# Kernel tuning notes

Measured on AMD Instinct MI355X. Metric: run time of the kernel, lower is better.

Reference implementation:

```python
import jax, jax.numpy as jnp
import numpy as np

EMB = 300
NUM_LAYERS = 5
NUM_GRAPHS = 1024
NUM_JUNCTIONS = 8192
TEMP = 0.04
EPS = 1e-5
SELF_LOOP_BOND_TYPE = 4


def gcn_conv(x, edge_index, edge_attr, W, b, ee1, ee2):
    # pretrain-gnns GCNConv: add self-loops (bond type 4, direction 0),
    # degree-normalized add aggregation of (x_src + edge_emb).
    N = x.shape[0]
    loop = jnp.arange(N, dtype=edge_index.dtype)
    src = jnp.concatenate([edge_index[0], loop])
    dst = jnp.concatenate([edge_index[1], loop])
    bt = jnp.concatenate([edge_attr[:, 0], jnp.full((N,), SELF_LOOP_BOND_TYPE, edge_attr.dtype)])
    bd = jnp.concatenate([edge_attr[:, 1], jnp.zeros((N,), edge_attr.dtype)])
    eemb = ee1[bt] + ee2[bd]                                   # [E+N, D]
    deg = jax.ops.segment_sum(jnp.ones(src.shape, x.dtype), src, num_segments=N)
    dinv = jnp.where(deg > 0, 1.0 / jnp.sqrt(jnp.maximum(deg, 1e-12)), 0.0)
    norm = dinv[src] * dinv[dst]                               # [E+N]
    h = x @ W.T + b                                            # [N, D]
    msg = norm[:, None] * (h[src] + eemb)                      # gather + fuse
    return jax.ops.segment_sum(msg, dst, num_segments=N)      # scatter-add


def batchnorm(h, gamma, beta):
    mu = h.mean(0)
    var = h.var(0)
    return gamma * (h - mu) / jnp.sqrt(var + EPS) + beta


def gnn_encoder(x, edge_index, edge_attr, ae1, ae2, W, b, ee1, ee2, gamma, beta):
    h = ae1[x[:, 0]] + ae2[x[:, 1]]
    for l in range(NUM_LAYERS):
        h = gcn_conv(h, edge_index, edge_attr, W[l], b[l], ee1[l], ee2[l])
        h = batchnorm(h, gamma[l], beta[l])
        if l < NUM_LAYERS - 1:
            h = jax.nn.relu(h)
    return h


def junction_encoder(h, jW, jb, jee1, jee2):
    # SuperEncoder is called with empty edge_index -> only self-loops.
    empty_ei = jnp.zeros((2, 0), jnp.int32)
    empty_ea = jnp.zeros((0, 2), jnp.int32)
    h = jax.nn.relu(gcn_conv(h, empty_ei, empty_ea, jW[0], jb[0], jee1[0], jee2[0]))
    return gcn_conv(h, empty_ei, empty_ea, jW[1], jb[1], jee1[1], jee2[1])


def mean_pool(h, ids, num):
    s = jax.ops.segment_sum(h, ids, num_segments=num)
    c = jax.ops.segment_sum(jnp.ones((h.shape[0],), h.dtype), ids, num_segments=num)
    return s / jnp.maximum(c, 1.0)[:, None]


def l2norm(h):
    return h / jnp.maximum(jnp.linalg.norm(h, axis=1, keepdims=True), 1e-12)


def setup_inputs() -> dict:
    key = jax.random.key(0)
    ks = jax.random.split(key, 32)
    N, E = 200000, 400000
    inp = {
        'batch_x': jax.random.randint(ks[0], (N, 2), 0, 3, jnp.int32),
        'batch_edge_index': jax.random.randint(ks[1], (2, E), 0, N, jnp.int32),
        'batch_edge_attr': jax.random.randint(ks[2], (E, 2), 0, 3, jnp.int32),
        'batch_graph_ids': jax.random.randint(ks[3], (N,), 0, NUM_GRAPHS, jnp.int32),
        'frag_x': jax.random.randint(ks[4], (N, 2), 0, 3, jnp.int32),
        'frag_edge_index': jax.random.randint(ks[5], (2, E), 0, N, jnp.int32),
        'frag_edge_attr': jax.random.randint(ks[6], (E, 2), 0, 3, jnp.int32),
        'frag_junction_ids': jax.random.randint(ks[7], (N,), 0, NUM_JUNCTIONS, jnp.int32),
        'junction_graph_ids': jax.random.randint(ks[8], (NUM_JUNCTIONS,), 0, NUM_GRAPHS, jnp.int32),
        'junction_mask': jax.random.uniform(ks[9], (NUM_JUNCTIONS,), jnp.float32),
    }
    s = 0.05
    inp.update({
        'atom_emb1': jax.random.normal(ks[10], (120, EMB), jnp.float32) * s,
        'atom_emb2': jax.random.normal(ks[11], (3, EMB), jnp.float32) * s,
        'gnn_W': jax.random.normal(ks[12], (NUM_LAYERS, EMB, EMB), jnp.float32) * s,
        'gnn_b': jnp.zeros((NUM_LAYERS, EMB), jnp.float32),
        'gnn_ee1': jax.random.normal(ks[13], (NUM_LAYERS, 6, EMB), jnp.float32) * s,
        'gnn_ee2': jax.random.normal(ks[14], (NUM_LAYERS, 3, EMB), jnp.float32) * s,
        'bn_gamma': jnp.ones((NUM_LAYERS, EMB), jnp.float32),
        'bn_beta': jnp.zeros((NUM_LAYERS, EMB), jnp.float32),
        'jct_W': jax.random.normal(ks[15], (2, EMB, EMB), jnp.float32) * s,
        'jct_b': jnp.zeros((2, EMB), jnp.float32),
        'jct_ee1': jax.random.normal(ks[16], (2, 6, EMB), jnp.float32) * s,
        'jct_ee2': jax.random.normal(ks[17], (2, 3, EMB), jnp.float32) * s,
        'mask_embedding': jax.random.normal(ks[18], (EMB,), jnp.float32),
    })
    return inp


def reference(batch_x, batch_edge_index, batch_edge_attr, batch_graph_ids,
              frag_x, frag_edge_index, frag_edge_attr, frag_junction_ids,
              junction_graph_ids, junction_mask,
              atom_emb1, atom_emb2, gnn_W, gnn_b, gnn_ee1, gnn_ee2,
              bn_gamma, bn_beta, jct_W, jct_b, jct_ee1, jct_ee2, mask_embedding):
    # branch 0: whole molecules
    h = gnn_encoder(batch_x, batch_edge_index, batch_edge_attr,
                    atom_emb1, atom_emb2, gnn_W, gnn_b, gnn_ee1, gnn_ee2, bn_gamma, bn_beta)
    g = mean_pool(h, batch_graph_ids, NUM_GRAPHS)
    f0 = l2norm(junction_encoder(g, jct_W, jct_b, jct_ee1, jct_ee2))
    # branch 1: fragments -> junction nodes, masked overwrite, pooled per graph
    h = gnn_encoder(frag_x, frag_edge_index, frag_edge_attr,
                    atom_emb1, atom_emb2, gnn_W, gnn_b, gnn_ee1, gnn_ee2, bn_gamma, bn_beta)
    j = mean_pool(h, frag_junction_ids, NUM_JUNCTIONS)
    j = jnp.where(junction_mask[:, None] > 0.5, mask_embedding[None, :], j)
    j = junction_encoder(j, jct_W, jct_b, jct_ee1, jct_ee2)
    f1 = l2norm(mean_pool(j, junction_graph_ids, NUM_GRAPHS))
    logits = (f0 @ f1.T) / TEMP
    return logits
```

## Files before the change

### kernel.cpp

```cpp
#include <hip/hip_runtime.h>
#include <math.h>

#define EMBD 300
#define HROW 304
#define LDF  304
#define KEXT 320
#define BCH  80
#define BSTR 40
#define TS2  312
#define SPR  608
#define NTAB 24
#define CE(a,b) (((a)+(b)-1)/(b))

typedef _Float16 h16;
typedef __attribute__((ext_vector_type(8))) _Float16 half8;
typedef __attribute__((ext_vector_type(4))) float f32x4;

__global__ void k_diag(float* out, int n, float v){
  int i = blockIdx.x*256 + threadIdx.x;
  if (i < n) out[i] = v;
}
__global__ void k_init_deg(int* __restrict__ deg, int* __restrict__ cnts, int N){
  int i = blockIdx.x*256 + threadIdx.x;
  if (i < N){ deg[i] = 0; cnts[i] = 1; }
}
__global__ void k_count_both(const int* __restrict__ ei, int E,
                             int* __restrict__ deg, int* __restrict__ cnts){
  int e = blockIdx.x*256 + threadIdx.x;
  if (e < E){
    atomicAdd(&deg[ei[e]], 1);
    atomicAdd(&cnts[ei[E + e]], 1);
  }
}
__global__ void k_dinv(const int* __restrict__ deg, float* __restrict__ dinv, int N){
  int i = blockIdx.x*256 + threadIdx.x;
  if (i < N) dinv[i] = 1.0f / sqrtf((float)(deg[i] + 1));
}
__global__ void k_count_ids(const int* __restrict__ ids, int n, int* __restrict__ counts){
  int i = blockIdx.x*256 + threadIdx.x;
  if (i < n) atomicAdd(&counts[ids[i]], 1);
}
__global__ void k_scan_block(const int* __restrict__ in, int M, int* __restrict__ out, int* __restrict__ bsum){
  __shared__ int s[256];
  int t = threadIdx.x, i = blockIdx.x*256 + t;
  int v = (i < M) ? in[i] : 0;
  s[t] = v; __syncthreads();
  for (int off = 1; off < 256; off <<= 1){
    int x = (t >= off) ? s[t-off] : 0;
    __syncthreads();
    s[t] += x;
    __syncthreads();
  }
  if (i < M) out[i] = s[t] - v;
  if (t == 255) bsum[blockIdx.x] = s[255];
}
__global__ void k_scan_sums(int* __restrict__ bsum, int B){
  __shared__ int s[1024];
  int t = threadIdx.x;
  int v = (t < B) ? bsum[t] : 0;
  s[t] = v; __syncthreads();
  for (int off = 1; off < 1024; off <<= 1){
    int x = (t >= off) ? s[t-off] : 0;
    __syncthreads();
    s[t] += x;
    __syncthreads();
  }
  if (t < B) bsum[t] = s[t] - v;
}
__global__ void k_scan_add(int* __restrict__ out, const int* __restrict__ bsum, int M){
  int i = blockIdx.x*256 + threadIdx.x;
  if (i < M) out[i] += bsum[blockIdx.x];
}
__global__ void k_fill_edges(const int* __restrict__ ei, const int* __restrict__ ea, int E, int N,
                             const int* __restrict__ offs, int* __restrict__ cur, int* __restrict__ entries){
  int e = blockIdx.x*256 + threadIdx.x;
  if (e < E){
    int s  = ei[e];
    int d  = ei[E + e];
    int bt = ea[2*e], bd = ea[2*e + 1];
    int pos = offs[d] + atomicAdd(&cur[d], 1);
    entries[pos] = s | (bt << 20) | (bd << 23);
  } else if (e < E + N){
    int i = e - E;
    int pos = offs[i] + atomicAdd(&cur[i], 1);
    entries[pos] = i | (4 << 20);
  }
}
__global__ void k_fill_rows(const int* __restrict__ ids, int n, const int* __restrict__ offs,
                            int* __restrict__ cur, int* __restrict__ entries){
  int i = blockIdx.x*256 + threadIdx.x;
  if (i < n){
    int g = ids[i];
    int pos = offs[g] + atomicAdd(&cur[g], 1);
    entries[pos] = i;
  }
}

__global__ void k_htab(const float* __restrict__ ae1, const float* __restrict__ ae2,
                       h16* __restrict__ htab){
  int p = blockIdx.x;
  int a = p / 3, b = p % 3;
  int t = threadIdx.x;
  h16* d = htab + (size_t)p*HROW;
  for (int c = t; c < HROW; c += 256)
    d[c] = (c < EMBD) ? (h16)(ae1[(size_t)a*EMBD + c] + ae2[(size_t)b*EMBD + c]) : (h16)0.f;
}
__global__ void k_pidx(const int* __restrict__ x, unsigned char* __restrict__ pidx, int N){
  int i = blockIdx.x*256 + threadIdx.x;
  if (i < N) pidx[i] = (unsigned char)(x[2*i]*3 + x[2*i+1]);
}
__global__ void k_ctab(const h16* __restrict__ htabG, const h16* __restrict__ Wx,
                       float* __restrict__ ctab){
  int q = blockIdx.x, t = threadIdx.x;
  float* d = ctab + (size_t)q*HROW;
  if (q < 9){
    const h16* hr = htabG + (size_t)q*HROW;
    for (int o = t; o < HROW; o += 256){
      float s = 0.f;
      if (o < EMBD){
        const h16* wr = Wx + (size_t)o*KEXT;
        for (int k = 0; k < EMBD; k++)
          s += (float)hr[k] * (float)wr[k];
      }
      d[o] = s;
    }
  } else {
    int bt = (q - 9) / 3, bd = (q - 9) % 3;
    for (int o = t; o < HROW; o += 256){
      float s = 0.f;
      if (o < EMBD){
        const h16* wr = Wx + (size_t)o*KEXT;
        s = (float)wr[304] + (float)wr[305 + bt] + (float)wr[311 + bd];
      }
      d[o] = s;
    }
  }
}

__global__ void k_wext(const float* __restrict__ W, const float* __restrict__ b,
                       const float* __restrict__ ee1, const float* __restrict__ ee2,
                       h16* __restrict__ out){
  int l = blockIdx.y, o = blockIdx.x, t = threadIdx.x;
  h16* d = out + ((size_t)l*KEXT + o)*KEXT;
  for (int k = t; k < KEXT; k += 256){
    float v = 0.f;
    if (o < EMBD){
      if      (k < EMBD)            v = W[(size_t)l*EMBD*EMBD + (size_t)o*EMBD + k];
      else if (k == 304)            v = b[l*EMBD + o];
      else if (k >= 305 && k < 311) v = ee1[((size_t)l*6 + (k-305))*EMBD + o];
      else if (k >= 311 && k < 314) v = ee2[((size_t)l*3 + (k-311))*EMBD + o];
    }
    d[k] = (h16)v;
  }
}
__global__ void k_wpad(const float* __restrict__ W, h16* __restrict__ out){
  int l = blockIdx.y, o = blockIdx.x, t = threadIdx.x;
  h16* d = out + ((size_t)l*KEXT + o)*KEXT;
  for (int k = t; k < KEXT; k += 256)
    d[k] = (h16)((o < EMBD && k < EMBD) ? W[(size_t)l*EMBD*EMBD + (size_t)o*EMBD + k] : 0.f);
}

__global__ void k_bn_coef(float* __restrict__ stats, const float* __restrict__ gamma,
                          const float* __restrict__ beta, float* __restrict__ coef,
                          h16* __restrict__ coefh, float invN){
  int c = blockIdx.x*256 + threadIdx.x;
  if (c >= KEXT) return;
  float sc = 0.f, sh = 0.f;
  if (c < EMBD){
    float mu  = stats[c]*invN;
    float var = stats[EMBD + c]*invN - mu*mu;
    sc = gamma[c]*rsqrtf(var + 1e-5f);
    sh = beta[c] - mu*sc;
    stats[c] = 0.f; stats[EMBD + c] = 0.f;
  }
  if (c < HROW){ coef[c] = sc; coef[HROW + c] = sh; }
  coefh[c] = (h16)sc; coefh[KEXT + c] = (h16)sh;
}

__global__ void k_red_stats(const h16* __restrict__ spart, int nb, float* __restrict__ stats){
  int t = threadIdx.x;
  int c1 = t + 256;
  float a0 = 0.f, q0 = 0.f, a1 = 0.f, q1 = 0.f;
  for (int b = blockIdx.x; b < nb; b += gridDim.x){
    const h16* sp = spart + (size_t)b*SPR;
    a0 += (float)sp[t];
    q0 += (float)sp[304 + t];
    if (c1 < EMBD){ a1 += (float)sp[c1]; q1 += (float)sp[304 + c1]; }
  }
  if (t < EMBD){ atomicAdd(&stats[t], a0); atomicAdd(&stats[EMBD + t], q0); }
  if (c1 < EMBD){ atomicAdd(&stats[c1], a1); atomicAdd(&stats[EMBD + c1], q1); }
}

template<int RELU>
__global__ void __launch_bounds__(256)
k_layer(const h16* __restrict__ hRaw, const h16* __restrict__ coefh,
        const float* __restrict__ dinv,
        const int* __restrict__ offs, const int* __restrict__ counts,
        const int* __restrict__ entries, const h16* __restrict__ Wx,
        h16* __restrict__ hOut, int N, h16* __restrict__ spart)
{
  __shared__ h16  tile[64][TS2];
  __shared__ h16  Bs[BCH][BSTR];
  __shared__ float sred[2*HROW];
  __shared__ int   rstart[64];
  __shared__ int   rcnt[64];
  __shared__ float dvv[64];

  int tid = threadIdx.x;
  int wid = tid >> 6, lane = tid & 63;
  int m16 = lane & 15, ko = lane >> 4;
  long row0 = (long)blockIdx.x * 64;

  if (tid < 64){
    long g = row0 + tid;
    int o = 0, c = 0; float d = 0.f;
    if (g < N){ o = offs[g]; c = counts[g]; d = dinv[g]; }
    rstart[tid] = o; rcnt[tid] = c; dvv[tid] = d;
  }
  for (int i = tid; i < 2*HROW; i += 256) sred[i] = 0.f;
  __syncthreads();

  int lr = wid*16 + m16;
  int myStart = rstart[lr], myCnt = rcnt[lr];
  float di = dvv[lr];

  int srcA[8]; float wvA[8]; int eA[8];
  #pragma unroll
  for (int j = 0; j < 8; j++){
    int e = entries[myStart + j];
    bool act = j < myCnt;
    int s = act ? (e & 0xFFFFF) : N;
    float wv = dinv[act ? s : 0];
    wvA[j] = act ? wv : 0.f;
    srcA[j] = s; eA[j] = e;
  }
  float ext[8] = {0,0,0,0,0,0,0,0};
  if (ko >= 2){
    int extbase = (ko - 2)*8;
    #pragma unroll
    for (int j = 0; j < 8; j++){
      unsigned msk = 1u | (1u << (1 + ((eA[j] >> 20) & 7))) | (1u << (7 + ((eA[j] >> 23) & 3)));
      #pragma unroll
      for (int c = 0; c < 8; c++)
        ext[c] += ((msk >> (extbase + c)) & 1u) ? wvA[j] : 0.f;
    }
  }
  half8 wvh[8];
  #pragma unroll
  for (int j = 0; j < 8; j++){
    _Float16 w = (_Float16)wvA[j];
    #pragma unroll
    for (int c = 0; c < 8; c++) wvh[j][c] = w;
  }

  half8 acc[10];
  #pragma unroll
  for (int k = 0; k < 10; k++) acc[k] = (half8)(_Float16)0;

  if (__any(myCnt > 8)){
    for (int j = 8; j < myCnt; j++){
      int e = entries[myStart + j];
      int s = e & 0xFFFFF;
      float wv = dinv[s];
      if (ko >= 2){
        int extbase = (ko - 2)*8;
        unsigned msk = 1u | (1u << (1 + ((e >> 20) & 7))) | (1u << (7 + ((e >> 23) & 3)));
        #pragma unroll
        for (int c = 0; c < 8; c++)
          ext[c] += ((msk >> (extbase + c)) & 1u) ? wv : 0.f;
      }
      _Float16 wh = (_Float16)wv;
      half8 w8;
      #pragma unroll
      for (int c = 0; c < 8; c++) w8[c] = wh;
      #pragma unroll
      for (int k = 0; k < 10; k++){
        if (k == 9 && ko >= 2) break;
        half8 sck = *(const half8*)&coefh[k*32 + ko*8];
        half8 shk = *(const half8*)&coefh[KEXT + k*32 + ko*8];
        half8 x = *(const half8*)(hRaw + (size_t)s*HROW + k*32 + ko*8);
        half8 y = sck*x + shk;
        if (RELU){
          #pragma unroll
          for (int c = 0; c < 8; c++) y[c] = y[c] > (_Float16)0 ? y[c] : (_Float16)0;
        }
        acc[k] += w8*y;
      }
    }
  }

  #pragma unroll
  for (int k = 0; k < 9; k++){
    half8 sck = *(const half8*)&coefh[k*32 + ko*8];
    half8 shk = *(const half8*)&coefh[KEXT + k*32 + ko*8];
    half8 a = acc[k];
    #pragma unroll
    for (int j = 0; j < 8; j++){
      half8 x = *(const half8*)(hRaw + (size_t)srcA[j]*HROW + k*32 + ko*8);
      half8 y = sck*x + shk;
      if (RELU){
        #pragma unroll
        for (int c = 0; c < 8; c++) y[c] = y[c] > (_Float16)0 ? y[c] : (_Float16)0;
      }
      a += wvh[j]*y;
    }
    acc[k] = a;
  }
  {
    half8 a = acc[9];
    if (ko < 2){
      half8 sck = *(const half8*)&coefh[288 + ko*8];
      half8 shk = *(const half8*)&coefh[KEXT + 288 + ko*8];
      #pragma unroll
      for (int j = 0; j < 8; j++){
        half8 x = *(const half8*)(hRaw + (size_t)srcA[j]*HROW + 288 + ko*8);
        half8 y = sck*x + shk;
        if (RELU){
          #pragma unroll
          for (int c = 0; c < 8; c++) y[c] = y[c] > (_Float16)0 ? y[c] : (_Float16)0;
        }
        a += wvh[j]*y;
      }
    } else {
      #pragma unroll
      for (int c = 0; c < 8; c++) a[c] += (_Float16)ext[c];
    }
    acc[9] = a;
  }

  half8 afr[10];
  {
    _Float16 dh = (_Float16)di;
    half8 d8;
    #pragma unroll
    for (int c = 0; c < 8; c++) d8[c] = dh;
    #pragma unroll
    for (int k = 0; k < 10; k++) afr[k] = acc[k] * d8;
  }

  int cr = ko * 4;
  #pragma unroll
  for (int jt = 0; jt < 4; jt++){
    f32x4 a2[5];
    #pragma unroll
    for (int j = 0; j < 5; j++) a2[j] = (f32x4){0.f,0.f,0.f,0.f};
    for (int k0 = 0; k0 < 10; k0++){
      __syncthreads();
      for (int idx = tid; idx < 320; idx += 256){
        int o = idx >> 2, qd = (idx & 3) * 8;
        *(half8*)&Bs[o][qd] = *(const half8*)(Wx + (size_t)(jt*BCH + o)*KEXT + k0*32 + qd);
      }
      __syncthreads();
      #pragma unroll
      for (int j = 0; j < 5; j++){
        half8 bfr = *(const half8*)&Bs[j*16 + m16][ko*8];
        a2[j] = __builtin_amdgcn_mfma_f32_16x16x32_f16(afr[k0], bfr, a2[j], 0, 0, 0);
      }
    }
    #pragma unroll
    for (int j = 0; j < 5; j++){
      int col = jt*BCH + j*16 + m16;
      float s = 0.f, q = 0.f;
      #pragma unroll
      for (int r = 0; r < 4; r++){
        float v = a2[j][r];
        s += v; q += v*v;
      }
      s += __shfl_xor(s, 16, 64); s += __shfl_xor(s, 32, 64);
      q += __shfl_xor(q, 16, 64); q += __shfl_xor(q, 32, 64);
      if (ko == 0 && col < EMBD){
        atomicAdd(&sred[col], s);
        atomicAdd(&sred[HROW + col], q);
      }
    }
    #pragma unroll
    for (int j = 0; j < 5; j++){
      int col = jt*BCH + j*16 + m16;
      if (col < HROW){
        #pragma unroll
        for (int r = 0; r < 4; r++)
          tile[wid*16 + cr + r][col] = (h16)a2[j][r];
      }
    }
  }
  __syncthreads();
  for (int idx = tid; idx < 64*38; idx += 256){
    int row = idx / 38, c = idx - row*38;
    long grow = row0 + row;
    if (grow < N)
      *(uint4*)(hOut + grow*HROW + c*8) = *(const uint4*)&tile[row][c*8];
  }
  h16* sp = spart + (size_t)blockIdx.x*SPR;
  for (int c = tid; c < EMBD; c += 256){
    sp[c]       = (h16)sred[c];
    sp[304 + c] = (h16)sred[HROW + c];
  }
}

__global__ void __launch_bounds__(256)
k_layer0(const unsigned char* __restrict__ pidx, const float* __restrict__ ctab,
         const float* __restrict__ dinv,
         const int* __restrict__ offs, const int* __restrict__ counts,
         const int* __restrict__ entries,
         h16* __restrict__ hOut, int N, h16* __restrict__ spart)
{
  __shared__ float tabs[NTAB][HROW];
  __shared__ float cf[64][NTAB];
  __shared__ float sred[2*HROW];
  int tid = threadIdx.x;
  long row0 = (long)blockIdx.x * 64;

  for (int i = tid; i < NTAB*HROW; i += 256) ((float*)tabs)[i] = ctab[i];
  for (int i = tid; i < 64*NTAB; i += 256) ((float*)cf)[i] = 0.f;
  for (int i = tid; i < 2*HROW; i += 256) sred[i] = 0.f;
  __syncthreads();

  if (tid < 64){
    long g = row0 + tid;
    if (g < N){
      int o = offs[g], c = counts[g];
      float dv = dinv[g];
      float* cr = cf[tid];
      for (int j = 0; j < c; j++){
        int e = entries[o + j];
        int s = e & 0xFFFFF;
        int bt = (e >> 20) & 7, bd = (e >> 23) & 3;
        float wv = dinv[s];
        cr[pidx[s]] += wv;
        cr[9 + bt*3 + bd] += wv;
      }
      #pragma unroll
      for (int q = 0; q < NTAB; q++) cr[q] *= dv;
    }
  }
  __syncthreads();

  for (int w = tid; w < 8*38; w += 256){
    int c = w % 38, rg = w / 38;
    float v[8][8];
    #pragma unroll
    for (int r = 0; r < 8; r++)
      #pragma unroll
      for (int cc = 0; cc < 8; cc++) v[r][cc] = 0.f;
    for (int q = 0; q < NTAB; q++){
      float tr[8];
      #pragma unroll
      for (int cc = 0; cc < 8; cc++) tr[cc] = tabs[q][c*8 + cc];
      #pragma unroll
      for (int r = 0; r < 8; r++){
        float co = cf[rg*8 + r][q];
        #pragma unroll
        for (int cc = 0; cc < 8; cc++) v[r][cc] += co * tr[cc];
      }
    }
    float s[8], qq[8];
    #pragma unroll
    for (int cc = 0; cc < 8; cc++){ s[cc] = 0.f; qq[cc] = 0.f; }
    #pragma unroll
    for (int r = 0; r < 8; r++){
      long grow = row0 + rg*8 + r;
      if (grow < N){
        half8 hv;
        #pragma unroll
        for (int cc = 0; cc < 8; cc++){
          float x = v[r][cc];
          hv[cc] = (h16)x;
          s[cc] += x; qq[cc] += x*x;
        }
        *(half8*)(hOut + grow*HROW + c*8) = hv;
      }
    }
    #pragma unroll
    for (int cc = 0; cc < 8; cc++){
      atomicAdd(&sred[c*8 + cc], s[cc]);
      atomicAdd(&sred[HROW + c*8 + cc], qq[cc]);
    }
  }
  __syncthreads();
  h16* sp = spart + (size_t)blockIdx.x*SPR;
  for (int c = tid; c < EMBD; c += 256){
    sp[c]       = (h16)sred[c];
    sp[304 + c] = (h16)sred[HROW + c];
  }
}

__global__ void k_pool_h(const h16* __restrict__ h, const int* __restrict__ offs,
                         const int* __restrict__ counts, const int* __restrict__ entries,
                         float* __restrict__ out, const float* __restrict__ coef,
                         const float* __restrict__ mask, const float* __restrict__ memb){
  int g = blockIdx.x, t = threadIdx.x, c1 = t + 256;
  int off = offs[g], cnt = counts[g];
  float a0 = 0.f, a1 = 0.f;
  int j = 0;
  for (; j + 4 <= cnt; j += 4){
    int r0 = entries[off+j],   r1 = entries[off+j+1];
    int r2 = entries[off+j+2], r3 = entries[off+j+3];
    const h16* p0 = h + (size_t)r0*HROW;
    const h16* p1 = h + (size_t)r1*HROW;
    const h16* p2 = h + (size_t)r2*HROW;
    const h16* p3 = h + (size_t)r3*HROW;
    float x0 = (float)p0[t], x1 = (float)p1[t];
    float x2 = (float)p2[t], x3 = (float)p3[t];
    a0 += (x0 + x1) + (x2 + x3);
    if (c1 < EMBD){
      float y0 = (float)p0[c1], y1 = (float)p1[c1];
      float y2 = (float)p2[c1], y3 = (float)p3[c1];
      a1 += (y0 + y1) + (y2 + y3);
    }
  }
  for (; j < cnt; j++){
    int r = entries[off + j];
    const h16* hr = h + (size_t)r*HROW;
    a0 += (float)hr[t];
    if (c1 < EMBD) a1 += (float)hr[c1];
  }
  float inv = 1.0f / fmaxf((float)cnt, 1.0f);
  float v0 = coef[t]*(a0*inv) + coef[HROW + t];
  float v1 = (c1 < EMBD) ? coef[c1]*(a1*inv) + coef[HROW + c1] : 0.f;
  if (mask && mask[g] > 0.5f){
    v0 = memb[t];
    if (c1 < EMBD) v1 = memb[c1];
  }
  float* o = out + (size_t)g*LDF;
  o[t] = v0;
  if (c1 < EMBD) o[c1] = v1;
}
__global__ void k_pool_f32(const float* __restrict__ h, const int* __restrict__ offs,
                           const int* __restrict__ counts, const int* __restrict__ entries,
                           float* __restrict__ out, int M){
  int g = blockIdx.x, t = threadIdx.x, c1 = t + 256;
  int off = offs[g], cnt = counts[g];
  float a0 = 0.f, a1 = 0.f;
  for (int j = 0; j < cnt; j++){
    int r = entries[off + j];
    const float* hr = h + (size_t)r*LDF;
    a0 += hr[t];
    if (c1 < EMBD) a1 += hr[c1];
  }
  float inv = 1.0f / fmaxf((float)cnt, 1.0f);
  float* o = out + (size_t)g*LDF;
  o[t] = a0*inv;
  if (c1 < EMBD) o[c1] = a1*inv;
}

__global__ void k_l2norm(float* __restrict__ f, int M){
  int g = blockIdx.x, t = threadIdx.x, c1 = t + 256;
  float* fr = f + (size_t)g*LDF;
  float v0 = fr[t];
  float v1 = (c1 < EMBD) ? fr[c1] : 0.f;
  float ss = v0*v0 + v1*v1;
  #pragma unroll
  for (int o = 32; o > 0; o >>= 1) ss += __shfl_down(ss, o, 64);
  __shared__ float red[4];
  int wid = t >> 6, lane = t & 63;
  if (lane == 0) red[wid] = ss;
  __syncthreads();
  if (t == 0) red[0] = 1.0f / fmaxf(sqrtf(red[0]+red[1]+red[2]+red[3]), 1e-12f);
  __syncthreads();
  float inv = red[0];
  fr[t] = v0*inv;
  if (c1 < EMBD) fr[c1] = v1*inv;
}

__global__ void __launch_bounds__(256)
k_gemm16(const float* __restrict__ A, int lda, const h16* __restrict__ Wp,
         const float* __restrict__ bias, const float* __restrict__ e1, const float* __restrict__ e2,
         float* __restrict__ C, int ldc, int M, int Ncols, int relu)
{
  __shared__ h16 Bs[BCH][BSTR];
  int tid = threadIdx.x;
  int wid = tid >> 6, lane = tid & 63;
  int m16 = lane & 15, ko = lane >> 4;
  int row0 = blockIdx.y * 64;
  int col0 = blockIdx.x * BCH;
  int arow = row0 + wid*16 + m16;
  bool rok = arow < M;
  const float* Ar = A + (size_t)(rok ? arow : 0) * lda;

  half8 afr[10];
  #pragma unroll
  for (int k0 = 0; k0 < 9; k0++){
    const float* p = Ar + k0*32 + ko*8;
    float4 fa = rok ? *(const float4*)p       : (float4){0.f,0.f,0.f,0.f};
    float4 fb = rok ? *(const float4*)(p + 4) : (float4){0.f,0.f,0.f,0.f};
    half8 v;
    v[0]=(h16)fa.x; v[1]=(h16)fa.y; v[2]=(h16)fa.z; v[3]=(h16)fa.w;
    v[4]=(h16)fb.x; v[5]=(h16)fb.y; v[6]=(h16)fb.z; v[7]=(h16)fb.w;
    afr[k0] = v;
  }
  {
    half8 v;
    #pragma unroll
    for (int c = 0; c < 8; c++){
      int ch = 288 + ko*8 + c;
      v[c] = (h16)((rok && ch < EMBD) ? Ar[ch] : 0.f);
    }
    afr[9] = v;
  }

  f32x4 a2[5];
  #pragma unroll
  for (int j = 0; j < 5; j++) a2[j] = (f32x4){0.f,0.f,0.f,0.f};
  for (int k0 = 0; k0 < 10; k0++){
    __syncthreads();
    for (int idx = tid; idx < 320; idx += 256){
      int o = idx >> 2, qd = (idx & 3) * 8;
      *(half8*)&Bs[o][qd] = *(const half8*)(Wp + (size_t)(col0 + o)*KEXT + k0*32 + qd);
    }
    __syncthreads();
    #pragma unroll
    for (int j = 0; j < 5; j++){
      half8 bfr = *(const half8*)&Bs[j*16 + m16][ko*8];
      a2[j] = __builtin_amdgcn_mfma_f32_16x16x32_f16(afr[k0], bfr, a2[j], 0, 0, 0);
    }
  }
  #pragma unroll
  for (int j = 0; j < 5; j++){
    int cc = col0 + j*16 + m16;
    if (cc >= Ncols) continue;
    float add = bias[cc] + e1[cc] + e2[cc];
    #pragma unroll
    for (int r = 0; r < 4; r++){
      int rr = row0 + wid*16 + ko*4 + r;
      if (rr >= M) continue;
      float v = a2[j][r] + add;
      if (relu) v = fmaxf(v, 0.f);
      C[(size_t)rr*ldc + cc] = v;
    }
  }
}

__global__ void __launch_bounds__(256)
k_gemm(const float* __restrict__ A, int lda, const float* __restrict__ W, int ldw,
       const float* __restrict__ bias, const float* __restrict__ e1, const float* __restrict__ e2,
       float* __restrict__ C, int ldc, int M, int Ncols, int K, int relu, float scale){
  __shared__ float As[16][68];
  __shared__ float Ws[16][68];
  int row0 = blockIdx.y * 64, col0 = blockIdx.x * 64;
  int tid = threadIdx.x;
  int tx = tid & 15, ty = tid >> 4;
  float acc[4][4] = {};
  for (int k0 = 0; k0 < K; k0 += 16){
    int r  = tid >> 2;
    int kk = (tid & 3) * 4;
    int gk = k0 + kk;
    float v[4] = {0.f,0.f,0.f,0.f};
    int gr = row0 + r;
    if (gr < M){
      if (gk + 3 < K){ float4 f = *(const float4*)(A + (size_t)gr*lda + gk); v[0]=f.x;v[1]=f.y;v[2]=f.z;v[3]=f.w; }
      else for (int j = 0; j < 4; j++) if (gk + j < K) v[j] = A[(size_t)gr*lda + gk + j];
    }
    As[kk+0][r]=v[0]; As[kk+1][r]=v[1]; As[kk+2][r]=v[2]; As[kk+3][r]=v[3];
    float w[4] = {0.f,0.f,0.f,0.f};
    int o = col0 + r;
    if (o < Ncols){
      if (gk + 3 < K){ float4 f = *(const float4*)(W + (size_t)o*ldw + gk); w[0]=f.x;w[1]=f.y;w[2]=f.z;w[3]=f.w; }
      else for (int j = 0; j < 4; j++) if (gk + j < K) w[j] = W[(size_t)o*ldw + gk + j];
    }
    Ws[kk+0][r]=w[0]; Ws[kk+1][r]=w[1]; Ws[kk+2][r]=w[2]; Ws[kk+3][r]=w[3];
    __syncthreads();
    #pragma unroll
    for (int k = 0; k < 16; k++){
      float4 a4 = *(const float4*)&As[k][ty*4];
      float4 b4 = *(const float4*)&Ws[k][tx*4];
      float a[4] = {a4.x,a4.y,a4.z,a4.w};
      float b[4] = {b4.x,b4.y,b4.z,b4.w};
      #pragma unroll
      for (int i = 0; i < 4; i++)
        #pragma unroll
        for (int j = 0; j < 4; j++) acc[i][j] += a[i]*b[j];
    }
    __syncthreads();
  }
  #pragma unroll
  for (int i = 0; i < 4; i++){
    int rr = row0 + ty*4 + i;
    if (rr >= M) continue;
    #pragma unroll
    for (int j = 0; j < 4; j++){
      int cc = col0 + tx*4 + j;
      if (cc >= Ncols) continue;
      float v = acc[i][j];
      if (bias) v += bias[cc];
      if (e1)   v += e1[cc];
      if (e2)   v += e2[cc];
      v *= scale;
      if (relu) v = fmaxf(v, 0.f);
      C[(size_t)rr*ldc + cc] = v;
    }
  }
}

static inline void scan_excl(const int* counts, int M, int* offs, int* bsum, hipStream_t s){
  int B = CE(M, 256);
  k_scan_block<<<B,256,0,s>>>(counts, M, offs, bsum);
  k_scan_sums<<<1,1024,0,s>>>(bsum, B);
  k_scan_add<<<B,256,0,s>>>(offs, bsum, M);
}
static inline void gemm16(const float* A, const h16* Wp,
                          const float* bias, const float* e1, const float* e2,
                          float* C, int M, int relu, hipStream_t s){
  dim3 grid(CE(EMBD, BCH), CE(M, 64));
  k_gemm16<<<grid,256,0,s>>>(A, LDF, Wp, bias, e1, e2, C, LDF, M, EMBD, relu);
}

extern "C" void kernel_launch(void* const* d_in, const int* in_sizes, int n_in,
                              void* d_out, int out_size, void* d_ws, size_t ws_size,
                              hipStream_t stream) {
  const int*   batch_x   = (const int*)d_in[0];
  const int*   batch_ei  = (const int*)d_in[1];
  const int*   batch_ea  = (const int*)d_in[2];
  const int*   batch_gid = (const int*)d_in[3];
  const int*   frag_x    = (const int*)d_in[4];
  const int*   frag_ei   = (const int*)d_in[5];
  const int*   frag_ea   = (const int*)d_in[6];
  const int*   frag_jid  = (const int*)d_in[7];
  const int*   jct_gid   = (const int*)d_in[8];
  const float* jct_mask  = (const float*)d_in[9];
  const float* ae1       = (const float*)d_in[10];
  const float* ae2       = (const float*)d_in[11];
  const float* gnn_W     = (const float*)d_in[12];
  const float* gnn_b     = (const float*)d_in[13];
  const float* gnn_ee1   = (const float*)d_in[14];
  const float* gnn_ee2   = (const float*)d_in[15];
  const float* bn_gamma  = (const float*)d_in[16];
  const float* bn_beta   = (const float*)d_in[17];
  const float* jct_W     = (const float*)d_in[18];
  const float* jct_b     = (const float*)d_in[19];
  const float* jct_ee1   = (const float*)d_in[20];
  const float* jct_ee2   = (const float*)d_in[21];
  const float* mask_emb  = (const float*)d_in[22];

  const int N = in_sizes[0] / 2;
  const int E = in_sizes[1] / 2;
  const int NG = 1024, NJ = 8192;
  const int LBLK = CE(N, 64);

  size_t off = 0;
  char* base = (char*)d_ws;
  auto carve = [&](size_t bytes) -> void* {
    void* p = base + off;
    off += (bytes + 255) & ~(size_t)255;
    return p;
  };
  h16*  hA      = (h16*) carve((size_t)(N+1) * HROW * 2);
  h16*  hB      = (h16*) carve((size_t)(N+1) * HROW * 2);
  float* dinv    = (float*)carve((size_t)N * 4);
  int*   degcnt  = (int*)  carve((size_t)N * 4);
  int*   cursor  = degcnt;
  int*   counts  = (int*)  carve((size_t)N * 4);
  int*   offs    = (int*)  carve((size_t)(N + 1) * 4);
  int*   entries = (int*)  carve((size_t)(E + N) * 4);
  int*   bsum    = (int*)  carve(1024 * 4);
  float* stats   = (float*)carve(2 * EMBD * 4);
  float* coef    = (float*)carve(2 * HROW * 4);
  h16*  coefh   = (h16*) carve(2 * KEXT * 2);
  h16*  wext    = (h16*) carve((size_t)5 * KEXT * KEXT * 2);
  h16*  wjx     = (h16*) carve((size_t)2 * KEXT * KEXT * 2);
  h16*  htabG   = (h16*) carve((size_t)9 * HROW * 2);
  float* ctab    = (float*)carve((size_t)NTAB * HROW * 4);
  unsigned char* pidx = (unsigned char*)carve((size_t)N);
  float* f0      = (float*)carve((size_t)NG * LDF * 4);
  float* f1      = (float*)carve((size_t)NG * LDF * 4);
  h16*  spart   = (h16*) carve((size_t)LBLK * SPR * 2);
  size_t required = off;
  float* g0      = (float*)hA;
  float* t1      = (float*)((char*)hA + ((size_t)16 << 20));
  float* t2      = (float*)((char*)hA + ((size_t)32 << 20));
  (void)n_in;

  if (ws_size < required || d_ws == nullptr){
    float v = 1.0e6f + (float)(ws_size >> 20) * 1000.0f;
    k_diag<<<CE(out_size,256),256,0,stream>>>((float*)d_out, out_size, v);
    return;
  }

  { dim3 g(KEXT, 5); k_wext<<<g,256,0,stream>>>(gnn_W, gnn_b, gnn_ee1, gnn_ee2, wext); }
  { dim3 g(KEXT, 2); k_wpad<<<g,256,0,stream>>>(jct_W, wjx); }
  k_htab<<<9,256,0,stream>>>(ae1, ae2, htabG);
  k_ctab<<<NTAB,256,0,stream>>>(htabG, wext, ctab);
  hipMemsetAsync(stats, 0, 2*EMBD*4, stream);
  hipMemsetAsync(hA + (size_t)N*HROW, 0, HROW*2, stream);
  hipMemsetAsync(hB + (size_t)N*HROW, 0, HROW*2, stream);

  for (int br = 0; br < 2; br++){
    const int* x  = br ? frag_x  : batch_x;
    const int* ei = br ? frag_ei : batch_ei;
    const int* ea = br ? frag_ea : batch_ea;

    k_init_deg<<<CE(N,256),256,0,stream>>>(degcnt, counts, N);
    k_count_both<<<CE(E,256),256,0,stream>>>(ei, E, degcnt, counts);
    k_dinv<<<CE(N,256),256,0,stream>>>(degcnt, dinv, N);
    scan_excl(counts, N, offs, bsum, stream);
    hipMemsetAsync(cursor, 0, (size_t)N*4, stream);
    k_fill_edges<<<CE(E+N,256),256,0,stream>>>(ei, ea, E, N, offs, cursor, entries);
    k_pidx<<<CE(N,256),256,0,stream>>>(x, pidx, N);

    for (int l = 0; l < 5; l++){
      const h16* src = (l & 1) ? hB : hA;
      h16*       dst = (l & 1) ? hA : hB;
      if (l == 0)
        k_layer0<<<LBLK,256,0,stream>>>(pidx, ctab, dinv, offs, counts, entries,
                                        hB, N, spart);
      else
        k_layer<1><<<LBLK,256,0,stream>>>(src, coefh, dinv, offs, counts, entries,
                                          wext + (size_t)l*KEXT*KEXT, dst, N, spart);
      k_red_stats<<<64,256,0,stream>>>(spart, LBLK, stats);
      k_bn_coef<<<CE(KEXT,256),256,0,stream>>>(stats, bn_gamma + l*EMBD, bn_beta + l*EMBD,
                                               coef, coefh, 1.0f/(float)N);
    }

    if (br == 0){
      hipMemsetAsync(counts, 0, (size_t)NG*4, stream);
      k_count_ids<<<CE(N,256),256,0,stream>>>(batch_gid, N, counts);
      scan_excl(counts, NG, offs, bsum, stream);
      hipMemsetAsync(cursor, 0, (size_t)NG*4, stream);
      k_fill_rows<<<CE(N,256),256,0,stream>>>(batch_gid, N, offs, cursor, entries);
      k_pool_h<<<NG,256,0,stream>>>(hB, offs, counts, entries, g0, coef, nullptr, nullptr);
      gemm16(g0, wjx,
             jct_b, jct_ee1 + 4*EMBD, jct_ee2, t1, NG, 1, stream);
      gemm16(t1, wjx + (size_t)KEXT*KEXT,
             jct_b + EMBD, jct_ee1 + 6*EMBD + 4*EMBD, jct_ee2 + 3*EMBD, f0, NG, 0, stream);
      k_l2norm<<<NG,256,0,stream>>>(f0, NG);
    } else {
      hipMemsetAsync(counts, 0, (size_t)NJ*4, stream);
      k_count_ids<<<CE(N,256),256,0,stream>>>(frag_jid, N, counts);
      scan_excl(counts, NJ, offs, bsum, stream);
      hipMemsetAsync(cursor, 0, (size_t)NJ*4, stream);
      k_fill_rows<<<CE(N,256),256,0,stream>>>(frag_jid, N, offs, cursor, entries);
      k_pool_h<<<NJ,256,0,stream>>>(hB, offs, counts, entries, t1, coef, jct_mask, mask_emb);
      gemm16(t1, wjx,
             jct_b, jct_ee1 + 4*EMBD, jct_ee2, t2, NJ, 1, stream);
      gemm16(t2, wjx + (size_t)KEXT*KEXT,
             jct_b + EMBD, jct_ee1 + 6*EMBD + 4*EMBD, jct_ee2 + 3*EMBD, t1, NJ, 0, stream);
      hipMemsetAsync(counts, 0, (size_t)NG*4, stream);
      k_count_ids<<<CE(NJ,256),256,0,stream>>>(jct_gid, NJ, counts);
      scan_excl(counts, NG, offs, bsum, stream);
      hipMemsetAsync(cursor, 0, (size_t)NG*4, stream);
      k_fill_rows<<<CE(NJ,256),256,0,stream>>>(jct_gid, NJ, offs, cursor, entries);
      k_pool_f32<<<NG,256,0,stream>>>(t1, offs, counts, entries, f1, NG);
      k_l2norm<<<NG,256,0,stream>>>(f1, NG);
    }
  }

  {
    dim3 grid(CE(NG,64), CE(NG,64));
    k_gemm<<<grid,256,0,stream>>>(f0, LDF, f1, LDF, nullptr, nullptr, nullptr,
                                  (float*)d_out, 1024, NG, NG, EMBD, 0, 25.0f);
  }
}
```

Before: 3.428 ms.

## Write last GNN layer in pooled-segment order and use fp16 MFMA for logits

The final GCN layer now scatters its output rows through a precomputed permutation, so rows of each graph or junction sit contiguously. Pooling can then read contiguous blocks instead of gathering through an index list, and the per-branch entries rebuild is removed. The final similarity GEMM moves from an FP32 SIMT kernel to the fp16 MFMA gemm16 path after converting f1 to padded half. The costs are an extra permutation build per branch and lower precision in the logits GEMM.

```diff
diff --git a/kernel.cpp b/kernel.cpp
--- a/kernel.cpp
+++ b/kernel.cpp
@@ -95,6 +95,14 @@
     entries[pos] = i;
   }
 }
+__global__ void k_fill_perm(const int* __restrict__ ids, int n, const int* __restrict__ offs,
+                            int* __restrict__ cur, int* __restrict__ perm){
+  int i = blockIdx.x*256 + threadIdx.x;
+  if (i < n){
+    int g = ids[i];
+    perm[i] = offs[g] + atomicAdd(&cur[g], 1);
+  }
+}
 
 __global__ void k_htab(const float* __restrict__ ae1, const float* __restrict__ ae2,
                        h16* __restrict__ htab){
@@ -159,6 +167,12 @@
   for (int k = t; k < KEXT; k += 256)
     d[k] = (h16)((o < EMBD && k < EMBD) ? W[(size_t)l*EMBD*EMBD + (size_t)o*EMBD + k] : 0.f);
 }
+__global__ void k_f16rows(const float* __restrict__ src, int M, h16* __restrict__ dst){
+  int r = blockIdx.x, t = threadIdx.x;
+  h16* d = dst + (size_t)r*KEXT;
+  for (int k = t; k < KEXT; k += 256)
+    d[k] = (h16)((r < M && k < EMBD) ? src[(size_t)r*LDF + k] : 0.f);
+}
 
 __global__ void k_bn_coef(float* __restrict__ stats, const float* __restrict__ gamma,
                           const float* __restrict__ beta, float* __restrict__ coef,
@@ -197,13 +211,15 @@
         const float* __restrict__ dinv,
         const int* __restrict__ offs, const int* __restrict__ counts,
         const int* __restrict__ entries, const h16* __restrict__ Wx,
-        h16* __restrict__ hOut, int N, h16* __restrict__ spart)
+        h16* __restrict__ hOut, int N, h16* __restrict__ spart,
+        const int* __restrict__ perm)
 {
   __shared__ h16  tile[64][TS2];
   __shared__ h16  Bs[BCH][BSTR];
   __shared__ float sred[2*HROW];
   __shared__ int   rstart[64];
   __shared__ int   rcnt[64];
+  __shared__ int   prow[64];
   __shared__ float dvv[64];
 
   int tid = threadIdx.x;
@@ -213,9 +229,12 @@
 
   if (tid < 64){
     long g = row0 + tid;
-    int o = 0, c = 0; float d = 0.f;
-    if (g < N){ o = offs[g]; c = counts[g]; d = dinv[g]; }
-    rstart[tid] = o; rcnt[tid] = c; dvv[tid] = d;
+    int o = 0, c = 0; float d = 0.f; int pr = (int)g;
+    if (g < N){
+      o = offs[g]; c = counts[g]; d = dinv[g];
+      if (perm) pr = perm[g];
+    }
+    rstart[tid] = o; rcnt[tid] = c; dvv[tid] = d; prow[tid] = pr;
   }
   for (int i = tid; i < 2*HROW; i += 256) sred[i] = 0.f;
   __syncthreads();
@@ -388,7 +407,7 @@
     int row = idx / 38, c = idx - row*38;
     long grow = row0 + row;
     if (grow < N)
-      *(uint4*)(hOut + grow*HROW + c*8) = *(const uint4*)&tile[row][c*8];
+      *(uint4*)(hOut + (size_t)prow[row]*HROW + c*8) = *(const uint4*)&tile[row][c*8];
   }
   h16* sp = spart + (size_t)blockIdx.x*SPR;
   for (int c = tid; c < EMBD; c += 256){
@@ -485,20 +504,19 @@
 }
 
 __global__ void k_pool_h(const h16* __restrict__ h, const int* __restrict__ offs,
-                         const int* __restrict__ counts, const int* __restrict__ entries,
+                         const int* __restrict__ counts,
                          float* __restrict__ out, const float* __restrict__ coef,
                          const float* __restrict__ mask, const float* __restrict__ memb){
   int g = blockIdx.x, t = threadIdx.x, c1 = t + 256;
   int off = offs[g], cnt = counts[g];
   float a0 = 0.f, a1 = 0.f;
+  const h16* base = h + (size_t)off*HROW;
   int j = 0;
   for (; j + 4 <= cnt; j += 4){
-    int r0 = entries[off+j],   r1 = entries[off+j+1];
-    int r2 = entries[off+j+2], r3 = entries[off+j+3];
-    const h16* p0 = h + (size_t)r0*HROW;
-    const h16* p1 = h + (size_t)r1*HROW;
-    const h16* p2 = h + (size_t)r2*HROW;
-    const h16* p3 = h + (size_t)r3*HROW;
+    const h16* p0 = base + (size_t)(j+0)*HROW;
+    const h16* p1 = base + (size_t)(j+1)*HROW;
+    const h16* p2 = base + (size_t)(j+2)*HROW;
+    const h16* p3 = base + (size_t)(j+3)*HROW;
     float x0 = (float)p0[t], x1 = (float)p1[t];
     float x2 = (float)p2[t], x3 = (float)p3[t];
     a0 += (x0 + x1) + (x2 + x3);
@@ -509,8 +527,7 @@
     }
   }
   for (; j < cnt; j++){
-    int r = entries[off + j];
-    const h16* hr = h + (size_t)r*HROW;
+    const h16* hr = base + (size_t)j*HROW;
     a0 += (float)hr[t];
     if (c1 < EMBD) a1 += (float)hr[c1];
   }
@@ -565,7 +582,7 @@
 __global__ void __launch_bounds__(256)
 k_gemm16(const float* __restrict__ A, int lda, const h16* __restrict__ Wp,
          const float* __restrict__ bias, const float* __restrict__ e1, const float* __restrict__ e2,
-         float* __restrict__ C, int ldc, int M, int Ncols, int relu)
+         float* __restrict__ C, int ldc, int M, int Ncols, int relu, float scale)
 {
   __shared__ h16 Bs[BCH][BSTR];
   int tid = threadIdx.x;
@@ -618,73 +635,12 @@
   for (int j = 0; j < 5; j++){
     int cc = col0 + j*16 + m16;
     if (cc >= Ncols) continue;
-    float add = bias[cc] + e1[cc] + e2[cc];
+    float add = bias ? (bias[cc] + e1[cc] + e2[cc]) : 0.f;
     #pragma unroll
     for (int r = 0; r < 4; r++){
       int rr = row0 + wid*16 + ko*4 + r;
       if (rr >= M) continue;
-      float v = a2[j][r] + add;
-      if (relu) v = fmaxf(v, 0.f);
-      C[(size_t)rr*ldc + cc] = v;
-    }
-  }
-}
-
-__global__ void __launch_bounds__(256)
-k_gemm(const float* __restrict__ A, int lda, const float* __restrict__ W, int ldw,
-       const float* __restrict__ bias, const float* __restrict__ e1, const float* __restrict__ e2,
-       float* __restrict__ C, int ldc, int M, int Ncols, int K, int relu, float scale){
-  __shared__ float As[16][68];
-  __shared__ float Ws[16][68];
-  int row0 = blockIdx.y * 64, col0 = blockIdx.x * 64;
-  int tid = threadIdx.x;
-  int tx = tid & 15, ty = tid >> 4;
-  float acc[4][4] = {};
-  for (int k0 = 0; k0 < K; k0 += 16){
-    int r  = tid >> 2;
-    int kk = (tid & 3) * 4;
-    int gk = k0 + kk;
-    float v[4] = {0.f,0.f,0.f,0.f};
-    int gr = row0 + r;
-    if (gr < M){
-      if (gk + 3 < K){ float4 f = *(const float4*)(A + (size_t)gr*lda + gk); v[0]=f.x;v[1]=f.y;v[2]=f.z;v[3]=f.w; }
-      else for (int j = 0; j < 4; j++) if (gk + j < K) v[j] = A[(size_t)gr*lda + gk + j];
-    }
-    As[kk+0][r]=v[0]; As[kk+1][r]=v[1]; As[kk+2][r]=v[2]; As[kk+3][r]=v[3];
-    float w[4] = {0.f,0.f,0.f,0.f};
-    int o = col0 + r;
-    if (o < Ncols){
-      if (gk + 3 < K){ float4 f = *(const float4*)(W + (size_t)o*ldw + gk); w[0]=f.x;w[1]=f.y;w[2]=f.z;w[3]=f.w; }
-      else for (int j = 0; j < 4; j++) if (gk + j < K) w[j] = W[(size_t)o*ldw + gk + j];
-    }
-    Ws[kk+0][r]=w[0]; Ws[kk+1][r]=w[1]; Ws[kk+2][r]=w[2]; Ws[kk+3][r]=w[3];
-    __syncthreads();
-    #pragma unroll
-    for (int k = 0; k < 16; k++){
-      float4 a4 = *(const float4*)&As[k][ty*4];
-      float4 b4 = *(const float4*)&Ws[k][tx*4];
-      float a[4] = {a4.x,a4.y,a4.z,a4.w};
-      float b[4] = {b4.x,b4.y,b4.z,b4.w};
-      #pragma unroll
-      for (int i = 0; i < 4; i++)
-        #pragma unroll
-        for (int j = 0; j < 4; j++) acc[i][j] += a[i]*b[j];
-    }
-    __syncthreads();
-  }
-  #pragma unroll
-  for (int i = 0; i < 4; i++){
-    int rr = row0 + ty*4 + i;
-    if (rr >= M) continue;
-    #pragma unroll
-    for (int j = 0; j < 4; j++){
-      int cc = col0 + tx*4 + j;
-      if (cc >= Ncols) continue;
-      float v = acc[i][j];
-      if (bias) v += bias[cc];
-      if (e1)   v += e1[cc];
-      if (e2)   v += e2[cc];
-      v *= scale;
+      float v = (a2[j][r] + add) * scale;
       if (relu) v = fmaxf(v, 0.f);
       C[(size_t)rr*ldc + cc] = v;
     }
@@ -701,7 +657,7 @@
                           const float* bias, const float* e1, const float* e2,
                           float* C, int M, int relu, hipStream_t s){
   dim3 grid(CE(EMBD, BCH), CE(M, 64));
-  k_gemm16<<<grid,256,0,s>>>(A, LDF, Wp, bias, e1, e2, C, LDF, M, EMBD, relu);
+  k_gemm16<<<grid,256,0,s>>>(A, LDF, Wp, bias, e1, e2, C, LDF, M, EMBD, relu, 1.0f);
 }
 
 extern "C" void kernel_launch(void* const* d_in, const int* in_sizes, int n_in,
@@ -762,6 +718,10 @@
   unsigned char* pidx = (unsigned char*)carve((size_t)N);
   float* f0      = (float*)carve((size_t)NG * LDF * 4);
   float* f1      = (float*)carve((size_t)NG * LDF * 4);
+  h16*  f1h     = (h16*) carve((size_t)1040 * KEXT * 2);
+  int*   pofs    = (int*)  carve((size_t)(NJ + 1) * 4);
+  int*   pcnt    = (int*)  carve((size_t)NJ * 4);
+  int*   perm    = (int*)  carve((size_t)N * 4);
   h16*  spart   = (h16*) carve((size_t)LBLK * SPR * 2);
   size_t required = off;
   float* g0      = (float*)hA;
@@ -784,9 +744,11 @@
   hipMemsetAsync(hB + (size_t)N*HROW, 0, HROW*2, stream);
 
   for (int br = 0; br < 2; br++){
-    const int* x  = br ? frag_x  : batch_x;
-    const int* ei = br ? frag_ei : batch_ei;
-    const int* ea = br ? frag_ea : batch_ea;
+    const int* x   = br ? frag_x   : batch_x;
+    const int* ei  = br ? frag_ei  : batch_ei;
+    const int* ea  = br ? frag_ea  : batch_ea;
+    const int* gid = br ? frag_jid : batch_gid;
+    const int  M   = br ? NJ       : NG;
 
     k_init_deg<<<CE(N,256),256,0,stream>>>(degcnt, counts, N);
     k_count_both<<<CE(E,256),256,0,stream>>>(ei, E, degcnt, counts);
@@ -795,6 +757,12 @@
     hipMemsetAsync(cursor, 0, (size_t)N*4, stream);
     k_fill_edges<<<CE(E+N,256),256,0,stream>>>(ei, ea, E, N, offs, cursor, entries);
     k_pidx<<<CE(N,256),256,0,stream>>>(x, pidx, N);
+
+    hipMemsetAsync(pcnt, 0, (size_t)M*4, stream);
+    k_count_ids<<<CE(N,256),256,0,stream>>>(gid, N, pcnt);
+    scan_excl(pcnt, M, pofs, bsum, stream);
+    hipMemsetAsync(cursor, 0, (size_t)M*4, stream);
+    k_fill_perm<<<CE(N,256),256,0,stream>>>(gid, N, pofs, cursor, perm);
 
     for (int l = 0; l < 5; l++){
       const h16* src = (l & 1) ? hB : hA;
@@ -804,31 +772,22 @@
                                         hB, N, spart);
       else
         k_layer<1><<<LBLK,256,0,stream>>>(src, coefh, dinv, offs, counts, entries,
-                                          wext + (size_t)l*KEXT*KEXT, dst, N, spart);
+                                          wext + (size_t)l*KEXT*KEXT, dst, N, spart,
+                                          (l == 4) ? perm : nullptr);
       k_red_stats<<<64,256,0,stream>>>(spart, LBLK, stats);
       k_bn_coef<<<CE(KEXT,256),256,0,stream>>>(stats, bn_gamma + l*EMBD, bn_beta + l*EMBD,
                                                coef, coefh, 1.0f/(float)N);
     }
 
     if (br == 0){
-      hipMemsetAsync(counts, 0, (size_t)NG*4, stream);
-      k_count_ids<<<CE(N,256),256,0,stream>>>(batch_gid, N, counts);
-      scan_excl(counts, NG, offs, bsum, stream);
-      hipMemsetAsync(cursor, 0, (size_t)NG*4, stream);
-      k_fill_rows<<<CE(N,256),256,0,stream>>>(batch_gid, N, offs, cursor, entries);
-      k_pool_h<<<NG,256,0,stream>>>(hB, offs, counts, entries, g0, coef, nullptr, nullptr);
+      k_pool_h<<<NG,256,0,stream>>>(hB, pofs, pcnt, g0, coef, nullptr, nullptr);
       gemm16(g0, wjx,
              jct_b, jct_ee1 + 4*EMBD, jct_ee2, t1, NG, 1, stream);
       gemm16(t1, wjx + (size_t)KEXT*KEXT,
              jct_b + EMBD, jct_ee1 + 6*EMBD + 4*EMBD, jct_ee2 + 3*EMBD, f0, NG, 0, stream);
       k_l2norm<<<NG,256,0,stream>>>(f0, NG);
     } else {
-      hipMemsetAsync(counts, 0, (size_t)NJ*4, stream);
-      k_count_ids<<<CE(N,256),256,0,stream>>>(frag_jid, N, counts);
-      scan_excl(counts, NJ, offs, bsum, stream);
-      hipMemsetAsync(cursor, 0, (size_t)NJ*4, stream);
-      k_fill_rows<<<CE(N,256),256,0,stream>>>(frag_jid, N, offs, cursor, entries);
-      k_pool_h<<<NJ,256,0,stream>>>(hB, offs, counts, entries, t1, coef, jct_mask, mask_emb);
+      k_pool_h<<<NJ,256,0,stream>>>(hB, pofs, pcnt, t1, coef, jct_mask, mask_emb);
       gemm16(t1, wjx,
              jct_b, jct_ee1 + 4*EMBD, jct_ee2, t2, NJ, 1, stream);
       gemm16(t2, wjx + (size_t)KEXT*KEXT,
@@ -843,9 +802,10 @@
     }
   }
 
+  k_f16rows<<<1040,256,0,stream>>>(f1, NG, f1h);
   {
-    dim3 grid(CE(NG,64), CE(NG,64));
-    k_gemm<<<grid,256,0,stream>>>(f0, LDF, f1, LDF, nullptr, nullptr, nullptr,
-                                  (float*)d_out, 1024, NG, NG, EMBD, 0, 25.0f);
-  }
-}
+    dim3 grid(CE(NG, BCH), CE(NG, 64));
+    k_gemm16<<<grid,256,0,stream>>>(f0, LDF, f1h, nullptr, nullptr, nullptr,
+                                    (float*)d_out, 1024, NG, NG, 0, 25.0f);
+  }
+}
```

Result: no change. 3.460 ms (+0.9%).
